# Kernel optimization log

Hardware: AMD Instinct MI355X
Metric: run time of the kernel (lower is better)

Reference implementation:

```python
import jax, jax.numpy as jnp
import numpy as np

GC = 128      # mem_dim
HEADS = 4     # gc / att_head_dim
HD = 32       # att_head_dim


def _dwconv(x, w, b, pad):
    # depthwise conv, NCHW, weight OIHW with I=1, groups=GC
    y = jax.lax.conv_general_dilated(
        x, w, window_strides=(1, 1),
        padding=((pad[0], pad[0]), (pad[1], pad[1])),
        feature_group_count=GC,
        dimension_numbers=('NCHW', 'OIHW', 'NCHW'))
    return y + b[None, :, None, None]


def setup_inputs() -> dict:
    key = jax.random.key(0)
    ks = jax.random.split(key, 5)
    x = jax.random.normal(ks[0], (32, 512, 56, 56), dtype=jnp.float32)
    w_dw1 = jax.random.normal(ks[1], (GC, 1, 3, 3), dtype=jnp.float32) * 0.1
    b_dw1 = jnp.zeros((GC,), jnp.float32)
    w_dw2 = jax.random.normal(ks[2], (GC, 1, 7, 7), dtype=jnp.float32) * 0.05
    b_dw2 = jnp.zeros((GC,), jnp.float32)
    w_qk = jax.random.normal(ks[3], (2 * GC, GC, 1, 1), dtype=jnp.float32) * (1.0 / np.sqrt(GC))
    b_qk = jnp.zeros((2 * GC,), jnp.float32)
    return {"x": x, "w_dw1": w_dw1, "b_dw1": b_dw1, "w_dw2": w_dw2,
            "b_dw2": b_dw2, "w_qk": w_qk, "b_qk": b_qk}


def reference(x, w_dw1, b_dw1, w_dw2, b_dw2, w_qk, b_qk):
    B, C, H, W = x.shape
    HW = H * W
    # grasp_memory + asymmetric_decouple (split along channels)
    m0 = C - 3 * GC
    mem = x[:, :m0]
    feat_att = x[:, m0:m0 + GC]
    feat_conv1 = x[:, m0 + GC:m0 + 2 * GC]
    feat_conv2 = x[:, m0 + 2 * GC:]
    feat_conv1 = _dwconv(feat_conv1, w_dw1, b_dw1, (1, 1))
    feat_conv2 = _dwconv(feat_conv2, w_dw2, b_dw2, (3, 3))
    # 1x1 conv qk -> [B, 2*GC, H, W]
    qk = jnp.einsum('bchw,oc->bohw', feat_att, w_qk[:, :, 0, 0]) + b_qk[None, :, None, None]
    qk = qk.reshape(B, 2 * GC, HW)
    q = qk[:, :GC].reshape(B, HEADS, HD, HW).transpose(0, 1, 3, 2)   # [B,h,HW,d]
    k = qk[:, GC:].reshape(B, HEADS, HD, HW).transpose(0, 1, 3, 2)
    v = feat_att.reshape(B, HEADS, HD, HW).transpose(0, 1, 3, 2)
    q = jax.nn.elu(q) + 1.0
    k = jax.nn.elu(k) + 1.0
    kmean = k.mean(axis=2, keepdims=True)                            # [B,h,1,d]
    z = 1.0 / (jnp.einsum('bhnd,bhmd->bhnm', q, kmean) + 1e-6)       # [B,h,HW,1]
    kv = jnp.einsum('bhnd,bhne->bhde', k, v) / HW                    # [B,h,d,d]
    att = jnp.einsum('bhnd,bhde->bhne', q, kv) * z                   # [B,h,HW,d]
    feat_att_out = att.transpose(0, 1, 3, 2).reshape(B, GC, H, W)
    feats = jnp.concatenate([feat_att_out, feat_conv1, feat_conv2], axis=1)
    return (mem, feats)
```

## Files before the change

### kernel.cpp

```cpp
#include <hip/hip_runtime.h>
#include <hip/hip_bf16.h>

#define Bn   32
#define Cn   512
#define GCn  128
#define HWn  3136
#define M0   128

#define Q_ELEMS  (Bn*GCn*HWn)
#define KV_ELEMS (Bn*4*32*32)
#define KS_ELEMS (Bn*4*32)

typedef __attribute__((ext_vector_type(8))) short bf16x8;
typedef __attribute__((ext_vector_type(4))) float f32x4;

__device__ __forceinline__ float bf2f(unsigned short u) {
    union { unsigned int i; float f; } v; v.i = ((unsigned int)u) << 16; return v.f;
}
__device__ __forceinline__ unsigned short f2bf(float f) {
    union { __hip_bfloat16 h; unsigned short u; } v; v.h = __float2bfloat16(f); return v.u;
}
__device__ __forceinline__ float act_elu1(float v) {
    return v > 0.0f ? v + 1.0f : __expf(v);
}

__global__ __launch_bounds__(256) void k_pre(
    const float* __restrict__ w_qk, unsigned short* __restrict__ wfrag,
    float* __restrict__ kvz) {
    const int t = threadIdx.x;
    if (blockIdx.x < 128) {
        int idx = blockIdx.x * 256 + t;
        int j  = idx & 7;
        int l  = (idx >> 3) & 63;
        int ks = (idx >> 9) & 3;
        int mt = idx >> 11;
        int o = mt * 16 + (l & 15);
        int c = ks * 32 + (l >> 4) * 8 + j;
        wfrag[idx] = f2bf(w_qk[o * 128 + c]);
    } else {
        int i = (blockIdx.x - 128) * 256 + t;
        kvz[i] = 0.0f;
    }
}

__device__ __forceinline__ void main_dev(
    const float* __restrict__ x, const unsigned short* __restrict__ wfrag,
    const float* __restrict__ b_qk,
    unsigned short* __restrict__ q_ws, float* __restrict__ kv_g,
    float* __restrict__ ks_g,
    unsigned short* Xn, unsigned short* Klds, int nt, int b) {

    unsigned short* Qlds = Xn;

    const int t  = threadIdx.x;
    const int n0 = nt * 64;
    const float* xa = x + ((long long)(b * Cn + M0)) * HWn;

    {
        const int c0 = t >> 1, half = t & 1;
        const float* src = xa + (long long)c0 * HWn + n0 + half * 32;
        #pragma unroll
        for (int p = 0; p < 8; ++p) {
            float4 v = *(const float4*)(src + p * 4);
            const int n = half * 32 + p * 4;
            Xn[(n + 0) * 144 + c0] = f2bf(v.x);
            Xn[(n + 1) * 144 + c0] = f2bf(v.y);
            Xn[(n + 2) * 144 + c0] = f2bf(v.z);
            Xn[(n + 3) * 144 + c0] = f2bf(v.w);
        }
    }
    __syncthreads();

    const int w = t >> 6, l = t & 63, nn = l & 15, q = l >> 4;
    f32x4 acc[4][4] = {};

    #pragma unroll
    for (int ks = 0; ks < 4; ++ks) {
        bf16x8 bq[4];
        #pragma unroll
        for (int in = 0; in < 4; ++in)
            bq[in] = *(const bf16x8*)(Xn + (in * 16 + nn) * 144 + ks * 32 + q * 8);
        #pragma unroll
        for (int im = 0; im < 4; ++im) {
            const int mt = 4 * w + im;
            bf16x8 aq = *(const bf16x8*)(wfrag + ((mt * 4 + ks) * 64 + l) * 8);
            #pragma unroll
            for (int in = 0; in < 4; ++in)
                acc[im][in] = __builtin_amdgcn_mfma_f32_16x16x32_bf16(aq, bq[in], acc[im][in], 0, 0, 0);
        }
    }

    if (w >= 2) {
        #pragma unroll
        for (int im = 0; im < 4; ++im) {
            const int obase = w * 64 + im * 16 + q * 4;
            float4 bias4 = *(const float4*)(b_qk + obase);
            const int krow = obase - 128;
            #pragma unroll
            for (int r = 0; r < 4; ++r) {
                const float bias = ((const float*)&bias4)[r];
                #pragma unroll
                for (int in = 0; in < 4; ++in)
                    Klds[(krow + r) * 72 + in * 16 + nn] = f2bf(act_elu1(acc[im][in][r] + bias));
            }
        }
    }
    __syncthreads();

    if (w < 2) {
        #pragma unroll
        for (int im = 0; im < 4; ++im) {
            const int obase = w * 64 + im * 16 + q * 4;
            float4 bias4 = *(const float4*)(b_qk + obase);
            #pragma unroll
            for (int r = 0; r < 4; ++r) {
                const float bias = ((const float*)&bias4)[r];
                #pragma unroll
                for (int in = 0; in < 4; ++in)
                    Qlds[(obase + r) * 72 + in * 16 + nn] = f2bf(act_elu1(acc[im][in][r] + bias));
            }
        }
    }

    {
        const int h = w;
        f32x4 akv[2][2] = {};
        float ksl0 = 0.0f, ksl1 = 0.0f;
        #pragma unroll
        for (int kt = 0; kt < 2; ++kt) {
            bf16x8 af0 = *(const bf16x8*)(Klds + (h * 32 + nn) * 72 + kt * 32 + q * 8);
            bf16x8 af1 = *(const bf16x8*)(Klds + (h * 32 + 16 + nn) * 72 + kt * 32 + q * 8);
            {
                const unsigned short* a0 = (const unsigned short*)&af0;
                const unsigned short* a1 = (const unsigned short*)&af1;
                #pragma unroll
                for (int j = 0; j < 8; ++j) { ksl0 += bf2f(a0[j]); ksl1 += bf2f(a1[j]); }
            }
            #pragma unroll
            for (int vt = 0; vt < 2; ++vt) {
                const float* vsrc = xa + (long long)(h * 32 + vt * 16 + nn) * HWn + n0 + kt * 32 + q * 8;
                float4 v0 = *(const float4*)(vsrc);
                float4 v1 = *(const float4*)(vsrc + 4);
                short tb[8];
                tb[0] = (short)f2bf(v0.x); tb[1] = (short)f2bf(v0.y);
                tb[2] = (short)f2bf(v0.z); tb[3] = (short)f2bf(v0.w);
                tb[4] = (short)f2bf(v1.x); tb[5] = (short)f2bf(v1.y);
                tb[6] = (short)f2bf(v1.z); tb[7] = (short)f2bf(v1.w);
                bf16x8 bv = *(bf16x8*)tb;
                akv[0][vt] = __builtin_amdgcn_mfma_f32_16x16x32_bf16(af0, bv, akv[0][vt], 0, 0, 0);
                akv[1][vt] = __builtin_amdgcn_mfma_f32_16x16x32_bf16(af1, bv, akv[1][vt], 0, 0, 0);
            }
        }
        const int bh = b * 4 + h;
        #pragma unroll
        for (int mt = 0; mt < 2; ++mt)
            #pragma unroll
            for (int vt = 0; vt < 2; ++vt)
                #pragma unroll
                for (int r = 0; r < 4; ++r)
                    atomicAdd(&kv_g[(bh << 10) + (mt * 16 + q * 4 + r) * 32 + vt * 16 + nn],
                              akv[mt][vt][r]);
        float s0 = ksl0; s0 += __shfl_xor(s0, 16, 64); s0 += __shfl_xor(s0, 32, 64);
        float s1 = ksl1; s1 += __shfl_xor(s1, 16, 64); s1 += __shfl_xor(s1, 32, 64);
        if (l < 16) {
            atomicAdd(&ks_g[bh * 32 + nn],      s0);
            atomicAdd(&ks_g[bh * 32 + 16 + nn], s1);
        }
    }
    __syncthreads();

    {
        const int row = t >> 1, hf = t & 1;
        const unsigned short* sp = Qlds + row * 72 + hf * 32;
        unsigned short* dp = q_ws + ((long long)(b * GCn + row)) * HWn + n0 + hf * 32;
        #pragma unroll
        for (int p = 0; p < 4; ++p)
            *(bf16x8*)(dp + p * 8) = *(const bf16x8*)(sp + p * 8);
    }
}

__global__ __launch_bounds__(256) void k_maincopy(
    const float* __restrict__ x, const unsigned short* __restrict__ wfrag,
    const float* __restrict__ b_qk,
    unsigned short* __restrict__ q_ws, float* __restrict__ kv_g,
    float* __restrict__ ks_g, float* __restrict__ mem_out) {

    __shared__ __align__(16) unsigned char smem[36864];
    const int bid = blockIdx.x;
    if (bid < 1568) {
        main_dev(x, wfrag, b_qk, q_ws, kv_g, ks_g,
                 (unsigned short*)smem, (unsigned short*)(smem + 18432),
                 bid % 49, bid / 49);
    } else {
        const int r = bid - 1568;
        for (int i4 = r * 256 + (int)threadIdx.x; i4 < 3211264; i4 += 2048 * 256) {
            int b  = i4 / 100352;
            int rr = i4 - b * 100352;
            ((float4*)mem_out)[i4] = ((const float4*)x)[(long long)b * 401408 + rr];
        }
    }
}

__device__ __forceinline__ void att_dev(
    const unsigned short* __restrict__ q_ws, const float* __restrict__ kv_g,
    const float* __restrict__ ks_g, float* __restrict__ feats,
    float* kvl, float* kml, int gx, int h, int b) {

    const int t = threadIdx.x;
    const int bh = b * 4 + h;
    const float inv = 1.0f / 3136.0f;
    #pragma unroll
    for (int p = 0; p < 4; ++p) kvl[t + p * 256] = kv_g[(bh << 10) + t + p * 256] * inv;
    if (t < 32) kml[t] = ks_g[bh * 32 + t] * inv;
    __syncthreads();

    const int n2 = gx * 256 + t;
    if (n2 >= 1568) return;
    const unsigned short* qp = q_ws + ((long long)(b * GCn + h * 32)) * HWn + n2 * 2;
    float a0[32], a1[32];
    float z0 = 1e-6f, z1 = 1e-6f;
    #pragma unroll
    for (int e = 0; e < 32; ++e) { a0[e] = 0.f; a1[e] = 0.f; }
    #pragma unroll 4
    for (int d = 0; d < 32; ++d) {
        const unsigned int qq = *(const unsigned int*)(qp + (long long)d * HWn);
        const float q0 = bf2f((unsigned short)qq);
        const float q1 = bf2f((unsigned short)(qq >> 16));
        z0 = __builtin_fmaf(q0, kml[d], z0);
        z1 = __builtin_fmaf(q1, kml[d], z1);
        #pragma unroll
        for (int e = 0; e < 32; ++e) {
            const float kv = kvl[d * 32 + e];
            a0[e] = __builtin_fmaf(q0, kv, a0[e]);
            a1[e] = __builtin_fmaf(q1, kv, a1[e]);
        }
    }
    z0 = 1.f / z0; z1 = 1.f / z1;
    float* op = feats + ((long long)(b * 384 + h * 32)) * HWn + n2 * 2;
    #pragma unroll
    for (int e = 0; e < 32; ++e)
        *(float2*)(op + (long long)e * HWn) = make_float2(a0[e] * z0, a1[e] * z1);
}

template<int KS, int PAD, int CIN>
__device__ __forceinline__ void dwconv2_dev(
    const float* __restrict__ x, const float* __restrict__ wg,
    const float* __restrict__ bg, float* __restrict__ feats,
    float* P, int cp, int b) {

    const int t = threadIdx.x;
    constexpr int ROWS = 56 + 2 * PAD;
    constexpr int PL = ROWS * 64;
    const int c0 = cp * 2;

    const float4 z4 = make_float4(0.f, 0.f, 0.f, 0.f);
    for (int i = t; i < (2 * PL) >> 2; i += 256) ((float4*)P)[i] = z4;
    __syncthreads();

    for (int i = t; i < 1568; i += 256) {
        const int ch = (i >= 784) ? 1 : 0;
        const int r  = i - ch * 784;
        const int y  = r / 14, k = r - y * 14;
        const float* in = x + ((long long)(b * Cn + CIN + c0 + ch)) * HWn + y * 56 + k * 4;
        const int row = y + PAD;
        const int ck  = (1 + k) ^ (row & 7);
        *(float4*)(P + ch * PL + row * 64 + ck * 4) = *(const float4*)in;
    }
    __syncthreads();

    for (int item = t; item < 392; item += 256) {
        const int ch = (item >= 196) ? 1 : 0;
        const int r  = item - ch * 196;
        const int ri = r / 7, m = r - ri * 7;
        const int y0 = ri * 2;
        const int xo = m * 8;
        const float* wp = wg + (c0 + ch) * KS * KS;
        const float bias = bg[c0 + ch];
        const float* Pc = P + ch * PL;
        float* op = feats + ((long long)(b * 384 + (CIN - 128) + c0 + ch)) * HWn;

        float a0[8], a1[8];
        #pragma unroll
        for (int j = 0; j < 8; ++j) { a0[j] = bias; a1[j] = bias; }
        #pragma unroll
        for (int dy = 0; dy <= KS; ++dy) {
            const int row = y0 + dy;
            float rr[16];
            #pragma unroll
            for (int u = 0; u < 4; ++u) {
                const int ck = ((xo >> 2) + u) ^ (row & 7);
                *(float4*)(rr + 4 * u) = *(const float4*)(Pc + row * 64 + ck * 4);
            }
            if (dy < KS) {
                #pragma unroll
                for (int dx = 0; dx < KS; ++dx) {
                    const float wv = wp[dy * KS + dx];
                    #pragma unroll
                    for (int j = 0; j < 8; ++j)
                        a0[j] = __builtin_fmaf(wv, rr[j + dx + 4 - PAD], a0[j]);
                }
            }
            if (dy >= 1) {
                #pragma unroll
                for (int dx = 0; dx < KS; ++dx) {
                    const float wv = wp[(dy - 1) * KS + dx];
                    #pragma unroll
                    for (int j = 0; j < 8; ++j)
                        a1[j] = __builtin_fmaf(wv, rr[j + dx + 4 - PAD], a1[j]);
                }
            }
        }
        *(float4*)(op + y0 * 56 + xo)           = make_float4(a0[0], a0[1], a0[2], a0[3]);
        *(float4*)(op + y0 * 56 + xo + 4)       = make_float4(a0[4], a0[5], a0[6], a0[7]);
        *(float4*)(op + (y0 + 1) * 56 + xo)     = make_float4(a1[0], a1[1], a1[2], a1[3]);
        *(float4*)(op + (y0 + 1) * 56 + xo + 4) = make_float4(a1[4], a1[5], a1[6], a1[7]);
    }
}

__global__ __launch_bounds__(256) void k_post2(
    const float* __restrict__ x,
    const unsigned short* __restrict__ q_ws, const float* __restrict__ kv_g,
    const float* __restrict__ ks_g,
    const float* __restrict__ w_dw1, const float* __restrict__ b_dw1,
    const float* __restrict__ w_dw2, const float* __restrict__ b_dw2,
    float* __restrict__ feats) {

    __shared__ __align__(16) float smem[2 * 62 * 64];
    const int bid = blockIdx.x;

    if (bid < 2048) {
        dwconv2_dev<7, 3, 384>(x, w_dw2, b_dw2, feats, smem, bid & 63, bid >> 6);
    } else if (bid < 4096) {
        const int r = bid - 2048;
        dwconv2_dev<3, 1, 256>(x, w_dw1, b_dw1, feats, smem, r & 63, r >> 6);
    } else {
        const int r = bid - 4096;
        const int b = r / 28, rem = r % 28;
        att_dev(q_ws, kv_g, ks_g, feats, smem, smem + 1024, rem % 7, rem / 7, b);
    }
}

extern "C" void kernel_launch(void* const* d_in, const int* in_sizes, int n_in,
                              void* d_out, int out_size, void* d_ws, size_t ws_size,
                              hipStream_t stream) {
    const float* x     = (const float*)d_in[0];
    const float* w_dw1 = (const float*)d_in[1];
    const float* b_dw1 = (const float*)d_in[2];
    const float* w_dw2 = (const float*)d_in[3];
    const float* b_dw2 = (const float*)d_in[4];
    const float* w_qk  = (const float*)d_in[5];
    const float* b_qk  = (const float*)d_in[6];
    float* out = (float*)d_out;

    unsigned short* q_ws = (unsigned short*)d_ws;
    float* kv_g = (float*)(q_ws + (long long)Q_ELEMS);
    float* ks_g = kv_g + KV_ELEMS;
    unsigned short* wfrag = (unsigned short*)(ks_g + KS_ELEMS);

    float* mem_out = out;
    float* feats   = out + (long long)Bn * GCn * HWn;

    k_pre     <<<656, 256, 0, stream>>>(w_qk, wfrag, kv_g);
    k_maincopy<<<3616, 256, 0, stream>>>(x, wfrag, b_qk, q_ws, kv_g, ks_g, mem_out);
    k_post2   <<<4992, 256, 0, stream>>>(x, q_ws, kv_g, ks_g,
                                         w_dw1, b_dw1, w_dw2, b_dw2, feats);
}
```

Baseline: 439.7 us.

## Process two spatial tiles per block and write Q directly from registers

Each block of the fused QK kernel now handles two 64-column tiles per batch. That halves the number of such blocks and the global atomics on kv/ksum, since accumulators stay in registers across tiles. The transposed X staging to LDS uses vectorized packed stores with an XOR swizzle to cut bank conflicts, and the MFMA operand order is swapped so Q can be written straight to global memory without an LDS round trip. The K column sums are taken from fp32 values before bf16 rounding, which slightly changes numerics. Fewer blocks may reduce parallelism and latency hiding.

```diff
diff --git a/kernel.cpp b/kernel.cpp
--- a/kernel.cpp
+++ b/kernel.cpp
@@ -48,134 +48,139 @@
     const float* __restrict__ b_qk,
     unsigned short* __restrict__ q_ws, float* __restrict__ kv_g,
     float* __restrict__ ks_g,
-    unsigned short* Xn, unsigned short* Klds, int nt, int b) {
-
-    unsigned short* Qlds = Xn;
+    unsigned short* Xn, unsigned short* Klds, int jb, int b) {
 
     const int t  = threadIdx.x;
-    const int n0 = nt * 64;
+    const int w  = t >> 6, l = t & 63, nn = l & 15, q = l >> 4;
     const float* xa = x + ((long long)(b * Cn + M0)) * HWn;
 
-    {
-        const int c0 = t >> 1, half = t & 1;
-        const float* src = xa + (long long)c0 * HWn + n0 + half * 32;
-        #pragma unroll
-        for (int p = 0; p < 8; ++p) {
-            float4 v = *(const float4*)(src + p * 4);
-            const int n = half * 32 + p * 4;
-            Xn[(n + 0) * 144 + c0] = f2bf(v.x);
-            Xn[(n + 1) * 144 + c0] = f2bf(v.y);
-            Xn[(n + 2) * 144 + c0] = f2bf(v.z);
-            Xn[(n + 3) * 144 + c0] = f2bf(v.w);
-        }
-    }
-    __syncthreads();
-
-    const int w = t >> 6, l = t & 63, nn = l & 15, q = l >> 4;
-    f32x4 acc[4][4] = {};
-
+    f32x4 akv[2][2] = {};
+    float ksp[4] = {0.f, 0.f, 0.f, 0.f};
+    const int ntile0 = jb * 2;
+    const int ntcnt  = (ntile0 + 1 < 49) ? 2 : 1;
+
+    for (int tt = 0; tt < ntcnt; ++tt) {
+        const int n0 = (ntile0 + tt) * 64;
+
+        {
+            const int c4 = (t & 31) * 4, no = t >> 5;
+            float rows[4][8];
+            #pragma unroll
+            for (int cc = 0; cc < 4; ++cc) {
+                *(float4*)(rows[cc])     = *(const float4*)(xa + (long long)(c4 + cc) * HWn + n0 + no * 8);
+                *(float4*)(rows[cc] + 4) = *(const float4*)(xa + (long long)(c4 + cc) * HWn + n0 + no * 8 + 4);
+            }
+            #pragma unroll
+            for (int i = 0; i < 8; ++i) {
+                const int n = no * 8 + i;
+                unsigned int lo = (unsigned int)f2bf(rows[0][i]) | ((unsigned int)f2bf(rows[1][i]) << 16);
+                unsigned int hi = (unsigned int)f2bf(rows[2][i]) | ((unsigned int)f2bf(rows[3][i]) << 16);
+                int off = (n * 144 + c4) * 2;
+                off ^= ((n & 7) << 4);
+                *(uint2*)((char*)Xn + off) = make_uint2(lo, hi);
+            }
+        }
+        __syncthreads();
+
+        f32x4 acc[4][4] = {};
+        #pragma unroll
+        for (int ks = 0; ks < 4; ++ks) {
+            bf16x8 bq[4];
+            #pragma unroll
+            for (int in = 0; in < 4; ++in) {
+                int off = ((in * 16 + nn) * 144 + ks * 32 + q * 8) * 2;
+                off ^= ((nn & 7) << 4);
+                bq[in] = *(const bf16x8*)((const char*)Xn + off);
+            }
+            #pragma unroll
+            for (int io = 0; io < 4; ++io) {
+                const int mt = 4 * w + io;
+                bf16x8 aq = *(const bf16x8*)(wfrag + ((mt * 4 + ks) * 64 + l) * 8);
+                #pragma unroll
+                for (int in = 0; in < 4; ++in)
+                    acc[in][io] = __builtin_amdgcn_mfma_f32_16x16x32_bf16(bq[in], aq, acc[in][io], 0, 0, 0);
+            }
+        }
+
+        if (w < 2) {
+            #pragma unroll
+            for (int io = 0; io < 4; ++io) {
+                const int o = w * 64 + io * 16 + nn;
+                const float bias = b_qk[o];
+                unsigned short* qb = q_ws + ((long long)(b * GCn + o)) * HWn + n0 + q * 4;
+                #pragma unroll
+                for (int in = 0; in < 4; ++in) {
+                    unsigned int lo = (unsigned int)f2bf(act_elu1(acc[in][io][0] + bias)) |
+                                      ((unsigned int)f2bf(act_elu1(acc[in][io][1] + bias)) << 16);
+                    unsigned int hi = (unsigned int)f2bf(act_elu1(acc[in][io][2] + bias)) |
+                                      ((unsigned int)f2bf(act_elu1(acc[in][io][3] + bias)) << 16);
+                    *(uint2*)(qb + in * 16) = make_uint2(lo, hi);
+                }
+            }
+        } else {
+            #pragma unroll
+            for (int io = 0; io < 4; ++io) {
+                const int krow = (w - 2) * 64 + io * 16 + nn;
+                const float bias = b_qk[128 + krow];
+                #pragma unroll
+                for (int in = 0; in < 4; ++in) {
+                    const float e0 = act_elu1(acc[in][io][0] + bias);
+                    const float e1 = act_elu1(acc[in][io][1] + bias);
+                    const float e2 = act_elu1(acc[in][io][2] + bias);
+                    const float e3 = act_elu1(acc[in][io][3] + bias);
+                    ksp[io] += (e0 + e1) + (e2 + e3);
+                    unsigned int lo = (unsigned int)f2bf(e0) | ((unsigned int)f2bf(e1) << 16);
+                    unsigned int hi = (unsigned int)f2bf(e2) | ((unsigned int)f2bf(e3) << 16);
+                    *(uint2*)(Klds + krow * 72 + in * 16 + q * 4) = make_uint2(lo, hi);
+                }
+            }
+        }
+        __syncthreads();
+
+        {
+            const int h = w;
+            #pragma unroll
+            for (int kt = 0; kt < 2; ++kt) {
+                bf16x8 af0 = *(const bf16x8*)(Klds + (h * 32 + nn) * 72 + kt * 32 + q * 8);
+                bf16x8 af1 = *(const bf16x8*)(Klds + (h * 32 + 16 + nn) * 72 + kt * 32 + q * 8);
+                #pragma unroll
+                for (int vt = 0; vt < 2; ++vt) {
+                    const float* vsrc = xa + (long long)(h * 32 + vt * 16 + nn) * HWn + n0 + kt * 32 + q * 8;
+                    float4 v0 = *(const float4*)(vsrc);
+                    float4 v1 = *(const float4*)(vsrc + 4);
+                    short tb[8];
+                    tb[0] = (short)f2bf(v0.x); tb[1] = (short)f2bf(v0.y);
+                    tb[2] = (short)f2bf(v0.z); tb[3] = (short)f2bf(v0.w);
+                    tb[4] = (short)f2bf(v1.x); tb[5] = (short)f2bf(v1.y);
+                    tb[6] = (short)f2bf(v1.z); tb[7] = (short)f2bf(v1.w);
+                    bf16x8 bv = *(bf16x8*)tb;
+                    akv[0][vt] = __builtin_amdgcn_mfma_f32_16x16x32_bf16(af0, bv, akv[0][vt], 0, 0, 0);
+                    akv[1][vt] = __builtin_amdgcn_mfma_f32_16x16x32_bf16(af1, bv, akv[1][vt], 0, 0, 0);
+                }
+            }
+        }
+    }
+
+    const int bh = b * 4 + w;
     #pragma unroll
-    for (int ks = 0; ks < 4; ++ks) {
-        bf16x8 bq[4];
-        #pragma unroll
-        for (int in = 0; in < 4; ++in)
-            bq[in] = *(const bf16x8*)(Xn + (in * 16 + nn) * 144 + ks * 32 + q * 8);
-        #pragma unroll
-        for (int im = 0; im < 4; ++im) {
-            const int mt = 4 * w + im;
-            bf16x8 aq = *(const bf16x8*)(wfrag + ((mt * 4 + ks) * 64 + l) * 8);
-            #pragma unroll
-            for (int in = 0; in < 4; ++in)
-                acc[im][in] = __builtin_amdgcn_mfma_f32_16x16x32_bf16(aq, bq[in], acc[im][in], 0, 0, 0);
-        }
-    }
-
+    for (int mt = 0; mt < 2; ++mt)
+        #pragma unroll
+        for (int vt = 0; vt < 2; ++vt)
+            #pragma unroll
+            for (int r = 0; r < 4; ++r)
+                atomicAdd(&kv_g[(bh << 10) + (mt * 16 + q * 4 + r) * 32 + vt * 16 + nn],
+                          akv[mt][vt][r]);
     if (w >= 2) {
         #pragma unroll
-        for (int im = 0; im < 4; ++im) {
-            const int obase = w * 64 + im * 16 + q * 4;
-            float4 bias4 = *(const float4*)(b_qk + obase);
-            const int krow = obase - 128;
-            #pragma unroll
-            for (int r = 0; r < 4; ++r) {
-                const float bias = ((const float*)&bias4)[r];
-                #pragma unroll
-                for (int in = 0; in < 4; ++in)
-                    Klds[(krow + r) * 72 + in * 16 + nn] = f2bf(act_elu1(acc[im][in][r] + bias));
-            }
-        }
-    }
-    __syncthreads();
-
-    if (w < 2) {
-        #pragma unroll
-        for (int im = 0; im < 4; ++im) {
-            const int obase = w * 64 + im * 16 + q * 4;
-            float4 bias4 = *(const float4*)(b_qk + obase);
-            #pragma unroll
-            for (int r = 0; r < 4; ++r) {
-                const float bias = ((const float*)&bias4)[r];
-                #pragma unroll
-                for (int in = 0; in < 4; ++in)
-                    Qlds[(obase + r) * 72 + in * 16 + nn] = f2bf(act_elu1(acc[im][in][r] + bias));
-            }
-        }
-    }
-
-    {
-        const int h = w;
-        f32x4 akv[2][2] = {};
-        float ksl0 = 0.0f, ksl1 = 0.0f;
-        #pragma unroll
-        for (int kt = 0; kt < 2; ++kt) {
-            bf16x8 af0 = *(const bf16x8*)(Klds + (h * 32 + nn) * 72 + kt * 32 + q * 8);
-            bf16x8 af1 = *(const bf16x8*)(Klds + (h * 32 + 16 + nn) * 72 + kt * 32 + q * 8);
-            {
-                const unsigned short* a0 = (const unsigned short*)&af0;
-                const unsigned short* a1 = (const unsigned short*)&af1;
-                #pragma unroll
-                for (int j = 0; j < 8; ++j) { ksl0 += bf2f(a0[j]); ksl1 += bf2f(a1[j]); }
-            }
-            #pragma unroll
-            for (int vt = 0; vt < 2; ++vt) {
-                const float* vsrc = xa + (long long)(h * 32 + vt * 16 + nn) * HWn + n0 + kt * 32 + q * 8;
-                float4 v0 = *(const float4*)(vsrc);
-                float4 v1 = *(const float4*)(vsrc + 4);
-                short tb[8];
-                tb[0] = (short)f2bf(v0.x); tb[1] = (short)f2bf(v0.y);
-                tb[2] = (short)f2bf(v0.z); tb[3] = (short)f2bf(v0.w);
-                tb[4] = (short)f2bf(v1.x); tb[5] = (short)f2bf(v1.y);
-                tb[6] = (short)f2bf(v1.z); tb[7] = (short)f2bf(v1.w);
-                bf16x8 bv = *(bf16x8*)tb;
-                akv[0][vt] = __builtin_amdgcn_mfma_f32_16x16x32_bf16(af0, bv, akv[0][vt], 0, 0, 0);
-                akv[1][vt] = __builtin_amdgcn_mfma_f32_16x16x32_bf16(af1, bv, akv[1][vt], 0, 0, 0);
-            }
-        }
-        const int bh = b * 4 + h;
-        #pragma unroll
-        for (int mt = 0; mt < 2; ++mt)
-            #pragma unroll
-            for (int vt = 0; vt < 2; ++vt)
-                #pragma unroll
-                for (int r = 0; r < 4; ++r)
-                    atomicAdd(&kv_g[(bh << 10) + (mt * 16 + q * 4 + r) * 32 + vt * 16 + nn],
-                              akv[mt][vt][r]);
-        float s0 = ksl0; s0 += __shfl_xor(s0, 16, 64); s0 += __shfl_xor(s0, 32, 64);
-        float s1 = ksl1; s1 += __shfl_xor(s1, 16, 64); s1 += __shfl_xor(s1, 32, 64);
-        if (l < 16) {
-            atomicAdd(&ks_g[bh * 32 + nn],      s0);
-            atomicAdd(&ks_g[bh * 32 + 16 + nn], s1);
-        }
-    }
-    __syncthreads();
-
-    {
-        const int row = t >> 1, hf = t & 1;
-        const unsigned short* sp = Qlds + row * 72 + hf * 32;
-        unsigned short* dp = q_ws + ((long long)(b * GCn + row)) * HWn + n0 + hf * 32;
-        #pragma unroll
-        for (int p = 0; p < 4; ++p)
-            *(bf16x8*)(dp + p * 8) = *(const bf16x8*)(sp + p * 8);
+        for (int io = 0; io < 4; ++io) {
+            float s = ksp[io];
+            s += __shfl_xor(s, 16, 64);
+            s += __shfl_xor(s, 32, 64);
+            if (q == 0) {
+                const int krow = (w - 2) * 64 + io * 16 + nn;
+                atomicAdd(&ks_g[b * 128 + krow], s);
+            }
+        }
     }
 }
 
@@ -187,12 +192,12 @@
 
     __shared__ __align__(16) unsigned char smem[36864];
     const int bid = blockIdx.x;
-    if (bid < 1568) {
+    if (bid < 800) {
         main_dev(x, wfrag, b_qk, q_ws, kv_g, ks_g,
                  (unsigned short*)smem, (unsigned short*)(smem + 18432),
-                 bid % 49, bid / 49);
+                 bid % 25, bid / 25);
     } else {
-        const int r = bid - 1568;
+        const int r = bid - 800;
         for (int i4 = r * 256 + (int)threadIdx.x; i4 < 3211264; i4 += 2048 * 256) {
             int b  = i4 / 100352;
             int rr = i4 - b * 100352;
@@ -361,7 +366,7 @@
     float* feats   = out + (long long)Bn * GCn * HWn;
 
     k_pre     <<<656, 256, 0, stream>>>(w_qk, wfrag, kv_g);
-    k_maincopy<<<3616, 256, 0, stream>>>(x, wfrag, b_qk, q_ws, kv_g, ks_g, mem_out);
+    k_maincopy<<<2848, 256, 0, stream>>>(x, wfrag, b_qk, q_ws, kv_g, ks_g, mem_out);
     k_post2   <<<4992, 256, 0, stream>>>(x, q_ws, kv_g, ks_g,
                                          w_dw1, b_dw1, w_dw2, b_dw2, feats);
 }
```

Result: slower. 452.1 us (+2.8%).

## Move depthwise convs into first fused kernel and isolate attention kernel

Applied to the files above, without the earlier changes.

The depthwise 3x3 and 7x7 conv blocks move out of the post kernel into the big first kernel. There they run alongside the QK projection and memory-copy blocks, while the attention output gets its own small kernel. The kv/ks zeroing is moved from k_pre to a hipMemsetAsync, so k_pre only converts weights. The goal is to overlap the independent conv work with the atomic-reduction stage and shrink the dependent tail kernel. The cost is a larger heterogeneous first grid plus one extra launch for the memset.

```diff
diff --git a/kernel.cpp b/kernel.cpp
--- a/kernel.cpp
+++ b/kernel.cpp
@@ -25,22 +25,15 @@
 }
 
 __global__ __launch_bounds__(256) void k_pre(
-    const float* __restrict__ w_qk, unsigned short* __restrict__ wfrag,
-    float* __restrict__ kvz) {
-    const int t = threadIdx.x;
-    if (blockIdx.x < 128) {
-        int idx = blockIdx.x * 256 + t;
-        int j  = idx & 7;
-        int l  = (idx >> 3) & 63;
-        int ks = (idx >> 9) & 3;
-        int mt = idx >> 11;
-        int o = mt * 16 + (l & 15);
-        int c = ks * 32 + (l >> 4) * 8 + j;
-        wfrag[idx] = f2bf(w_qk[o * 128 + c]);
-    } else {
-        int i = (blockIdx.x - 128) * 256 + t;
-        kvz[i] = 0.0f;
-    }
+    const float* __restrict__ w_qk, unsigned short* __restrict__ wfrag) {
+    int idx = blockIdx.x * 256 + threadIdx.x;
+    int j  = idx & 7;
+    int l  = (idx >> 3) & 63;
+    int ks = (idx >> 9) & 3;
+    int mt = idx >> 11;
+    int o = mt * 16 + (l & 15);
+    int c = ks * 32 + (l >> 4) * 8 + j;
+    wfrag[idx] = f2bf(w_qk[o * 128 + c]);
 }
 
 __device__ __forceinline__ void main_dev(
@@ -179,20 +172,105 @@
     }
 }
 
-__global__ __launch_bounds__(256) void k_maincopy(
+template<int KS, int PAD, int CIN>
+__device__ __forceinline__ void dwconv2_dev(
+    const float* __restrict__ x, const float* __restrict__ wg,
+    const float* __restrict__ bg, float* __restrict__ feats,
+    float* P, int cp, int b) {
+
+    const int t = threadIdx.x;
+    constexpr int ROWS = 56 + 2 * PAD;
+    constexpr int PL = ROWS * 64;
+    const int c0 = cp * 2;
+
+    const float4 z4 = make_float4(0.f, 0.f, 0.f, 0.f);
+    for (int i = t; i < (2 * PL) >> 2; i += 256) ((float4*)P)[i] = z4;
+    __syncthreads();
+
+    for (int i = t; i < 1568; i += 256) {
+        const int ch = (i >= 784) ? 1 : 0;
+        const int r  = i - ch * 784;
+        const int y  = r / 14, k = r - y * 14;
+        const float* in = x + ((long long)(b * Cn + CIN + c0 + ch)) * HWn + y * 56 + k * 4;
+        const int row = y + PAD;
+        const int ck  = (1 + k) ^ (row & 7);
+        *(float4*)(P + ch * PL + row * 64 + ck * 4) = *(const float4*)in;
+    }
+    __syncthreads();
+
+    for (int item = t; item < 392; item += 256) {
+        const int ch = (item >= 196) ? 1 : 0;
+        const int r  = item - ch * 196;
+        const int ri = r / 7, m = r - ri * 7;
+        const int y0 = ri * 2;
+        const int xo = m * 8;
+        const float* wp = wg + (c0 + ch) * KS * KS;
+        const float bias = bg[c0 + ch];
+        const float* Pc = P + ch * PL;
+        float* op = feats + ((long long)(b * 384 + (CIN - 128) + c0 + ch)) * HWn;
+
+        float a0[8], a1[8];
+        #pragma unroll
+        for (int j = 0; j < 8; ++j) { a0[j] = bias; a1[j] = bias; }
+        #pragma unroll
+        for (int dy = 0; dy <= KS; ++dy) {
+            const int row = y0 + dy;
+            float rr[16];
+            #pragma unroll
+            for (int u = 0; u < 4; ++u) {
+                const int ck = ((xo >> 2) + u) ^ (row & 7);
+                *(float4*)(rr + 4 * u) = *(const float4*)(Pc + row * 64 + ck * 4);
+            }
+            if (dy < KS) {
+                #pragma unroll
+                for (int dx = 0; dx < KS; ++dx) {
+                    const float wv = wp[dy * KS + dx];
+                    #pragma unroll
+                    for (int j = 0; j < 8; ++j)
+                        a0[j] = __builtin_fmaf(wv, rr[j + dx + 4 - PAD], a0[j]);
+                }
+            }
+            if (dy >= 1) {
+                #pragma unroll
+                for (int dx = 0; dx < KS; ++dx) {
+                    const float wv = wp[(dy - 1) * KS + dx];
+                    #pragma unroll
+                    for (int j = 0; j < 8; ++j)
+                        a1[j] = __builtin_fmaf(wv, rr[j + dx + 4 - PAD], a1[j]);
+                }
+            }
+        }
+        *(float4*)(op + y0 * 56 + xo)           = make_float4(a0[0], a0[1], a0[2], a0[3]);
+        *(float4*)(op + y0 * 56 + xo + 4)       = make_float4(a0[4], a0[5], a0[6], a0[7]);
+        *(float4*)(op + (y0 + 1) * 56 + xo)     = make_float4(a1[0], a1[1], a1[2], a1[3]);
+        *(float4*)(op + (y0 + 1) * 56 + xo + 4) = make_float4(a1[4], a1[5], a1[6], a1[7]);
+    }
+}
+
+__global__ __launch_bounds__(256) void k_big(
     const float* __restrict__ x, const unsigned short* __restrict__ wfrag,
     const float* __restrict__ b_qk,
     unsigned short* __restrict__ q_ws, float* __restrict__ kv_g,
-    float* __restrict__ ks_g, float* __restrict__ mem_out) {
+    float* __restrict__ ks_g,
+    const float* __restrict__ w_dw1, const float* __restrict__ b_dw1,
+    const float* __restrict__ w_dw2, const float* __restrict__ b_dw2,
+    float* __restrict__ mem_out, float* __restrict__ feats) {
 
     __shared__ __align__(16) unsigned char smem[36864];
     const int bid = blockIdx.x;
+
     if (bid < 1568) {
         main_dev(x, wfrag, b_qk, q_ws, kv_g, ks_g,
                  (unsigned short*)smem, (unsigned short*)(smem + 18432),
                  bid % 49, bid / 49);
+    } else if (bid < 3616) {
+        const int r = bid - 1568;
+        dwconv2_dev<7, 3, 384>(x, w_dw2, b_dw2, feats, (float*)smem, r & 63, r >> 6);
+    } else if (bid < 5664) {
+        const int r = bid - 3616;
+        dwconv2_dev<3, 1, 256>(x, w_dw1, b_dw1, feats, (float*)smem, r & 63, r >> 6);
     } else {
-        const int r = bid - 1568;
+        const int r = bid - 5664;
         for (int i4 = r * 256 + (int)threadIdx.x; i4 < 3211264; i4 += 2048 * 256) {
             int b  = i4 / 100352;
             int rr = i4 - b * 100352;
@@ -201,12 +279,16 @@
     }
 }
 
-__device__ __forceinline__ void att_dev(
+__global__ __launch_bounds__(256) void k_att(
     const unsigned short* __restrict__ q_ws, const float* __restrict__ kv_g,
-    const float* __restrict__ ks_g, float* __restrict__ feats,
-    float* kvl, float* kml, int gx, int h, int b) {
-
+    const float* __restrict__ ks_g, float* __restrict__ feats) {
+
+    __shared__ float kvl[1024];
+    __shared__ float kml[32];
     const int t = threadIdx.x;
+    const int r = blockIdx.x;
+    const int b = r / 28, rem = r % 28;
+    const int gx = rem % 7, h = rem / 7;
     const int bh = b * 4 + h;
     const float inv = 1.0f / 3136.0f;
     #pragma unroll
@@ -242,104 +324,6 @@
         *(float2*)(op + (long long)e * HWn) = make_float2(a0[e] * z0, a1[e] * z1);
 }
 
-template<int KS, int PAD, int CIN>
-__device__ __forceinline__ void dwconv2_dev(
-    const float* __restrict__ x, const float* __restrict__ wg,
-    const float* __restrict__ bg, float* __restrict__ feats,
-    float* P, int cp, int b) {
-
-    const int t = threadIdx.x;
-    constexpr int ROWS = 56 + 2 * PAD;
-    constexpr int PL = ROWS * 64;
-    const int c0 = cp * 2;
-
-    const float4 z4 = make_float4(0.f, 0.f, 0.f, 0.f);
-    for (int i = t; i < (2 * PL) >> 2; i += 256) ((float4*)P)[i] = z4;
-    __syncthreads();
-
-    for (int i = t; i < 1568; i += 256) {
-        const int ch = (i >= 784) ? 1 : 0;
-        const int r  = i - ch * 784;
-        const int y  = r / 14, k = r - y * 14;
-        const float* in = x + ((long long)(b * Cn + CIN + c0 + ch)) * HWn + y * 56 + k * 4;
-        const int row = y + PAD;
-        const int ck  = (1 + k) ^ (row & 7);
-        *(float4*)(P + ch * PL + row * 64 + ck * 4) = *(const float4*)in;
-    }
-    __syncthreads();
-
-    for (int item = t; item < 392; item += 256) {
-        const int ch = (item >= 196) ? 1 : 0;
-        const int r  = item - ch * 196;
-        const int ri = r / 7, m = r - ri * 7;
-        const int y0 = ri * 2;
-        const int xo = m * 8;
-        const float* wp = wg + (c0 + ch) * KS * KS;
-        const float bias = bg[c0 + ch];
-        const float* Pc = P + ch * PL;
-        float* op = feats + ((long long)(b * 384 + (CIN - 128) + c0 + ch)) * HWn;
-
-        float a0[8], a1[8];
-        #pragma unroll
-        for (int j = 0; j < 8; ++j) { a0[j] = bias; a1[j] = bias; }
-        #pragma unroll
-        for (int dy = 0; dy <= KS; ++dy) {
-            const int row = y0 + dy;
-            float rr[16];
-            #pragma unroll
-            for (int u = 0; u < 4; ++u) {
-                const int ck = ((xo >> 2) + u) ^ (row & 7);
-                *(float4*)(rr + 4 * u) = *(const float4*)(Pc + row * 64 + ck * 4);
-            }
-            if (dy < KS) {
-                #pragma unroll
-                for (int dx = 0; dx < KS; ++dx) {
-                    const float wv = wp[dy * KS + dx];
-                    #pragma unroll
-                    for (int j = 0; j < 8; ++j)
-                        a0[j] = __builtin_fmaf(wv, rr[j + dx + 4 - PAD], a0[j]);
-                }
-            }
-            if (dy >= 1) {
-                #pragma unroll
-                for (int dx = 0; dx < KS; ++dx) {
-                    const float wv = wp[(dy - 1) * KS + dx];
-                    #pragma unroll
-                    for (int j = 0; j < 8; ++j)
-                        a1[j] = __builtin_fmaf(wv, rr[j + dx + 4 - PAD], a1[j]);
-                }
-            }
-        }
-        *(float4*)(op + y0 * 56 + xo)           = make_float4(a0[0], a0[1], a0[2], a0[3]);
-        *(float4*)(op + y0 * 56 + xo + 4)       = make_float4(a0[4], a0[5], a0[6], a0[7]);
-        *(float4*)(op + (y0 + 1) * 56 + xo)     = make_float4(a1[0], a1[1], a1[2], a1[3]);
-        *(float4*)(op + (y0 + 1) * 56 + xo + 4) = make_float4(a1[4], a1[5], a1[6], a1[7]);
-    }
-}
-
-__global__ __launch_bounds__(256) void k_post2(
-    const float* __restrict__ x,
-    const unsigned short* __restrict__ q_ws, const float* __restrict__ kv_g,
-    const float* __restrict__ ks_g,
-    const float* __restrict__ w_dw1, const float* __restrict__ b_dw1,
-    const float* __restrict__ w_dw2, const float* __restrict__ b_dw2,
-    float* __restrict__ feats) {
-
-    __shared__ __align__(16) float smem[2 * 62 * 64];
-    const int bid = blockIdx.x;
-
-    if (bid < 2048) {
-        dwconv2_dev<7, 3, 384>(x, w_dw2, b_dw2, feats, smem, bid & 63, bid >> 6);
-    } else if (bid < 4096) {
-        const int r = bid - 2048;
-        dwconv2_dev<3, 1, 256>(x, w_dw1, b_dw1, feats, smem, r & 63, r >> 6);
-    } else {
-        const int r = bid - 4096;
-        const int b = r / 28, rem = r % 28;
-        att_dev(q_ws, kv_g, ks_g, feats, smem, smem + 1024, rem % 7, rem / 7, b);
-    }
-}
-
 extern "C" void kernel_launch(void* const* d_in, const int* in_sizes, int n_in,
                               void* d_out, int out_size, void* d_ws, size_t ws_size,
                               hipStream_t stream) {
@@ -360,8 +344,9 @@
     float* mem_out = out;
     float* feats   = out + (long long)Bn * GCn * HWn;
 
-    k_pre     <<<656, 256, 0, stream>>>(w_qk, wfrag, kv_g);
-    k_maincopy<<<3616, 256, 0, stream>>>(x, wfrag, b_qk, q_ws, kv_g, ks_g, mem_out);
-    k_post2   <<<4992, 256, 0, stream>>>(x, q_ws, kv_g, ks_g,
-                                         w_dw1, b_dw1, w_dw2, b_dw2, feats);
-}
+    hipMemsetAsync(kv_g, 0, (KV_ELEMS + KS_ELEMS) * sizeof(float), stream);
+    k_pre<<<128, 256, 0, stream>>>(w_qk, wfrag);
+    k_big<<<7712, 256, 0, stream>>>(x, wfrag, b_qk, q_ws, kv_g, ks_g,
+                                    w_dw1, b_dw1, w_dw2, b_dw2, mem_out, feats);
+    k_att<<<896, 256, 0, stream>>>(q_ws, kv_g, ks_g, feats);
+}
```

After: 461.8 us. 1.05x slower.
